# Optimization experiments

Hardware: AMD Instinct MI355X
Metric: run time of the kernel (lower is better)

## Reference

```python
import jax, jax.numpy as jnp
import numpy as np

NUM_CATEGORIES = 72
TEMPERATURE = 0.07
SEGMENT_WEIGHT = 10.0
MISSING_CATEGORIES = (13, 53, 61)
EPS = 1e-12
NEG_INF = -1e30


def setup_inputs() -> dict:
    key = jax.random.key(0)
    k1, k2 = jax.random.split(key)
    B, N, D = 4, 262144, 32
    embeddings = jax.random.normal(k1, (B, N, D), dtype=jnp.float32)
    segment_labels = jax.random.randint(k2, (B, N), 0, NUM_CATEGORIES, dtype=jnp.int64)
    return {"embeddings": embeddings, "segment_labels": segment_labels}


def _l2norm(x):
    return x / jnp.maximum(jnp.linalg.norm(x, axis=-1, keepdims=True), EPS)


def reference(embeddings, segment_labels):
    C = NUM_CATEGORIES
    missing = jnp.zeros((C,), dtype=bool).at[jnp.array(MISSING_CATEGORIES)].set(True)
    valid = segment_labels >= 0                      # [B,N]
    labels = jnp.clip(segment_labels, 0, C - 1)      # safe indices
    emb_n = _l2norm(embeddings)                      # [B,N,D]

    def per_batch(e, lab, v):
        w = v.astype(e.dtype)                                        # [N]
        counts = jax.ops.segment_sum(w, lab, num_segments=C)         # [C]
        sums = jax.ops.segment_sum(e * w[:, None], lab, num_segments=C)  # [C,D]
        protos = _l2norm(sums / jnp.maximum(counts, 1.0)[:, None])   # [C,D]
        present = (counts > 0) & (~missing)                          # [C]
        # similarity over all categories, mask absent/missing prototypes
        sim = jnp.einsum('nd,cd->nc', e, protos) / TEMPERATURE       # [N,C]
        logits = jnp.where(present[None, :], sim, NEG_INF)
        logp = jax.nn.log_softmax(logits, axis=-1)
        nll = -jnp.take_along_axis(logp, lab[:, None], axis=1)[:, 0]  # [N]
        keep = (v & (~missing[lab])).astype(e.dtype)                  # ignore_index=-100 analogue
        return jnp.sum(nll * keep) / jnp.maximum(jnp.sum(keep), 1.0)

    losses = jax.vmap(per_batch)(emb_n, labels, valid)  # [B]
    segment_loss = jnp.mean(losses)                     # segment_count == B here
    return SEGMENT_WEIGHT * segment_loss
```

## Files before the change

kernel.cpp:

```cpp
#include <hip/hip_runtime.h>
#include <hip/hip_bf16.h>

#define NCAT 72
#define NCATP 80
#define DIM 32
#define ROWS 36
#define BNUM 4
#define TEMP_INV (1.0f / 0.07f)
#define SEG_W 10.0f

#define WS_SUMS 0
#define WS_CNTS 9216
#define WS_PROT 9504
#define WS_NABS 19744
#define WS_LOSS 19748
#define WS_KEEP 19752
#define WS_TOTAL 19756

typedef __attribute__((ext_vector_type(8))) short short8v;
typedef __attribute__((ext_vector_type(4))) float f32x4;
typedef __attribute__((ext_vector_type(4))) unsigned u32x4;

__device__ __forceinline__ bool is_missing(int c) {
    return (c == 13) | (c == 53) | (c == 61);
}

__device__ __forceinline__ short f2bf_hi(float f, float* hi_f) {
    unsigned u = __float_as_uint(f);
    unsigned r = u + 0x7FFFu + ((u >> 16) & 1u);
    *hi_f = __uint_as_float(r & 0xFFFF0000u);
    return (short)(r >> 16);
}
__device__ __forceinline__ short f2bf(float f) {
    unsigned u = __float_as_uint(f);
    unsigned r = u + 0x7FFFu + ((u >> 16) & 1u);
    return (short)(r >> 16);
}

__device__ __forceinline__ unsigned cvtpk_bf16(float a, float b) {
    unsigned r;
    asm("v_cvt_pk_bf16_f32 %0, %1, %2" : "=v"(r) : "v"(a), "v"(b));
    return r;
}

template <int BPB>
__global__ __launch_bounds__(256) void k_accum(const float* __restrict__ emb,
                                               const int* __restrict__ lab,
                                               float* __restrict__ ws, int Nb) {
    __shared__ float s_acc[4][NCAT][ROWS];
    __shared__ float s_cnt[4][NCAT];
    __shared__ int   s_prb[4][NCAT];
    const int t = threadIdx.x;
    const int b = blockIdx.x / BPB;
    const int blk = blockIdx.x % BPB;
    const int w = t >> 6;
    const int g = (t >> 3) & 7;
    const int sub = t & 7;
    const int pofs = t >> 3;

    for (int i = t; i < 4 * NCAT * ROWS; i += 256) ((float*)s_acc)[i] = 0.f;
    for (int i = t; i < 4 * NCAT; i += 256) ((float*)s_cnt)[i] = 0.f;
    __syncthreads();

    float* accw = &s_acc[w][0][0];
    int* prbw = &s_prb[w][0];
    const float* eb = emb + (size_t)b * Nb * DIM;
    const int* lb = lab + (size_t)b * Nb;

    int p = blk * 32 + pofs;
    int l_cur = lb[p];
    float4 v_cur = ((const float4*)(eb + (size_t)p * DIM))[sub];

    for (int p0 = blk * 32; p0 < Nb; p0 += BPB * 32) {
        const int pn = p0 + BPB * 32 + pofs;
        int l_nxt = -1;
        float4 v_nxt = make_float4(0.f, 0.f, 0.f, 0.f);
        if (pn < Nb) {
            l_nxt = lb[pn];
            v_nxt = ((const float4*)(eb + (size_t)pn * DIM))[sub];
        }

        float ss = v_cur.x * v_cur.x + v_cur.y * v_cur.y +
                   v_cur.z * v_cur.z + v_cur.w * v_cur.w;
        ss += __shfl_xor(ss, 1);
        ss += __shfl_xor(ss, 2);
        ss += __shfl_xor(ss, 4);
        const float inv = 1.0f / fmaxf(sqrtf(ss), 1e-12f);
        const bool valid = (l_cur >= 0);
        const int lc = min(max(l_cur, 0), NCAT - 1);
        float4 u;
        u.x = v_cur.x * inv; u.y = v_cur.y * inv;
        u.z = v_cur.z * inv; u.w = v_cur.w * inv;

        if (valid && sub == 0) unsafeAtomicAdd(&s_cnt[w][lc], 1.0f);

        float* rowp = accw + lc * ROWS + sub * 4;
        bool active = valid;
        while (__any(active)) {
            asm volatile("" ::: "memory");
            if (active && sub == 0) prbw[lc] = g;
            int win = 0;
            if (active && sub == 0) win = (prbw[lc] == g) ? 1 : 0;
            const unsigned long long wb = __ballot(win);
            const bool iwin = active && ((wb >> (g * 8)) & 1ull);
            if (iwin) {
                float4* r4 = (float4*)rowp;
                float4 o = *r4;
                o.x += u.x; o.y += u.y; o.z += u.z; o.w += u.w;
                *r4 = o;
            }
            active = active && !iwin;
        }

        l_cur = l_nxt;
        v_cur = v_nxt;
    }
    __syncthreads();

    float* gs = ws + WS_SUMS + b * NCAT * DIM;
    for (int i = t; i < NCAT * DIM; i += 256) {
        const int c = i >> 5, d = i & 31;
        float val = s_acc[0][c][d] + s_acc[1][c][d] +
                    s_acc[2][c][d] + s_acc[3][c][d];
        if (val != 0.f) unsafeAtomicAdd(&gs[i], val);
    }
    if (t < NCAT) {
        float c = s_cnt[0][t] + s_cnt[1][t] + s_cnt[2][t] + s_cnt[3][t];
        if (c != 0.f) unsafeAtomicAdd(ws + WS_CNTS + b * NCAT + t, c);
    }
}

__global__ __launch_bounds__(256) void k_proto(float* __restrict__ ws) {
    const int b = blockIdx.x;
    __shared__ float s_np;
    if (threadIdx.x == 0) s_np = 0.f;
    __syncthreads();
    const float* gs = ws + WS_SUMS + b * NCAT * DIM;
    const float* gc = ws + WS_CNTS + b * NCAT;
    float* gp = ws + WS_PROT + b * NCATP * DIM;
    const int dd = threadIdx.x & 31;
    const int r0 = threadIdx.x >> 5;
    for (int c = r0; c < NCAT; c += 8) {
        float cnt = gc[c];
        float val = gs[c * DIM + dd] / fmaxf(cnt, 1.0f);
        float ss = val * val;
        #pragma unroll
        for (int m = 16; m >= 1; m >>= 1) ss += __shfl_xor(ss, m);
        float inv = 1.0f / fmaxf(sqrtf(ss), 1e-12f);
        const bool present = (cnt > 0.f) && !is_missing(c);
        gp[c * DIM + dd] = present ? val * inv : 0.f;
        if (dd == 0) unsafeAtomicAdd(&s_np, present ? 1.f : 0.f);
    }
    __syncthreads();
    if (threadIdx.x == 0) ws[WS_NABS + b] = (float)NCATP - s_np;
}

__device__ __forceinline__ void point_group(
    int pt, int l, const float* __restrict__ eb,
    const short8v phi[5], const short8v plo[5],
    float nabs, int sub, float& lacc, float& dacc, float& kacc)
{
    const float LOG2E = 1.4426950408889634f;
    const int lc = min(max(l, 0), NCAT - 1);

    const float4* ep = (const float4*)(eb + (size_t)pt * DIM + sub * 8);
    float4 a0 = ep[0], a1 = ep[1];

    float ea[8] = {a0.x, a0.y, a0.z, a0.w, a1.x, a1.y, a1.z, a1.w};
    u32x4 hw, lw;
    #pragma unroll
    for (int j = 0; j < 4; j++) {
        const float x0 = ea[2 * j], x1 = ea[2 * j + 1];
        const unsigned h = cvtpk_bf16(x0, x1);
        const float h0 = __uint_as_float(h << 16);
        const float h1 = __uint_as_float(h & 0xFFFF0000u);
        hw[j] = h;
        lw[j] = cvtpk_bf16(x0 - h0, x1 - h1);
    }
    const short8v ehi = __builtin_bit_cast(short8v, hw);
    const short8v elo = __builtin_bit_cast(short8v, lw);

    float ss = a0.x * a0.x + a0.y * a0.y + a0.z * a0.z + a0.w * a0.w +
               a1.x * a1.x + a1.y * a1.y + a1.z * a1.z + a1.w * a1.w;
    ss += __shfl_xor(ss, 16);
    ss += __shfl_xor(ss, 32);
    const float kk = (TEMP_INV * LOG2E) * __builtin_amdgcn_rsqf(fmaxf(ss, 1e-24f));

    const bool keep = (l >= 0) && !is_missing(lc);
    const int ltile = lc >> 4;
    const bool qm = keep && (((lc >> 2) & 3) == sub);

    float s = 0.f;
    #pragma unroll
    for (int n = 0; n < 5; n++) {
        f32x4 acc = {0.f, 0.f, 0.f, 0.f};
        acc = __builtin_amdgcn_mfma_f32_16x16x32_bf16(phi[n], ehi, acc, 0, 0, 0);
        acc = __builtin_amdgcn_mfma_f32_16x16x32_bf16(plo[n], ehi, acc, 0, 0, 0);
        acc = __builtin_amdgcn_mfma_f32_16x16x32_bf16(phi[n], elo, acc, 0, 0, 0);
        s += __builtin_amdgcn_exp2f(acc[0] * kk) + __builtin_amdgcn_exp2f(acc[1] * kk) +
             __builtin_amdgcn_exp2f(acc[2] * kk) + __builtin_amdgcn_exp2f(acc[3] * kk);
        if (qm && ltile == n) {
            const float d01 = (lc & 1) ? acc[1] : acc[0];
            const float d23 = (lc & 1) ? acc[3] : acc[2];
            dacc += kk * ((lc & 2) ? d23 : d01);
        }
    }
    s += __shfl_xor(s, 16);
    s += __shfl_xor(s, 32);
    s -= nabs;
    const float cl = __builtin_amdgcn_logf(s);
    if (keep && sub == 0) {
        lacc += cl;
        kacc += 1.f;
    }
}

template <int BPB>
__global__ __launch_bounds__(256, 4) void k_loss(const float* __restrict__ emb,
                                                 const int* __restrict__ lab,
                                                 const float* __restrict__ protos,
                                                 const float* __restrict__ nabsp,
                                                 float* __restrict__ lossout,
                                                 int Nb) {
    __shared__ float s_red[8];
    const int b = blockIdx.x / BPB;
    const int blk = blockIdx.x % BPB;
    const int t = threadIdx.x;
    const int lane = t & 63;
    const int wave = t >> 6;
    const int lid = lane & 15;
    const int sub = lane >> 4;

    const float* pp = protos + b * NCATP * DIM;
    const float nabs = nabsp[b];
    const float* eb = emb + (size_t)b * Nb * DIM;
    const int* lb = lab + (size_t)b * Nb;
    const float LN2 = 0.6931471805599453f;

    short8v phi[5], plo[5];
    #pragma unroll
    for (int n = 0; n < 5; n++) {
        const int cat = n * 16 + lid;
        const float4* qk = (const float4*)(pp + cat * DIM + sub * 8);
        float4 q0 = qk[0], q1 = qk[1];
        float qa[8] = {q0.x, q0.y, q0.z, q0.w, q1.x, q1.y, q1.z, q1.w};
        #pragma unroll
        for (int j = 0; j < 8; j++) {
            float hf;
            phi[n][j] = f2bf_hi(qa[j], &hf);
            plo[n][j] = f2bf(qa[j] - hf);
        }
    }

    float lacc = 0.f, dacc = 0.f, kacc = 0.f;

    #pragma unroll 1
    for (int p0 = (blk * 4 + wave) * 64; p0 < Nb; p0 += BPB * 4 * 64) {
        const int lv = lb[p0 + lane];
        const int l0 = __shfl(lv, lid);
        const int l1 = __shfl(lv, 16 + lid);
        const int l2 = __shfl(lv, 32 + lid);
        const int l3 = __shfl(lv, 48 + lid);
        point_group(p0 + lid,      l0, eb, phi, plo, nabs, sub, lacc, dacc, kacc);
        point_group(p0 + 16 + lid, l1, eb, phi, plo, nabs, sub, lacc, dacc, kacc);
        point_group(p0 + 32 + lid, l2, eb, phi, plo, nabs, sub, lacc, dacc, kacc);
        point_group(p0 + 48 + lid, l3, eb, phi, plo, nabs, sub, lacc, dacc, kacc);
    }

    float v = lacc - dacc;
    #pragma unroll
    for (int m = 32; m >= 1; m >>= 1) {
        v += __shfl_xor(v, m);
        kacc += __shfl_xor(kacc, m);
    }
    if (lane == 0) {
        s_red[wave] = v;
        s_red[4 + wave] = kacc;
    }
    __syncthreads();
    if (t == 0) {
        float a = s_red[0] + s_red[1] + s_red[2] + s_red[3];
        float k = s_red[4] + s_red[5] + s_red[6] + s_red[7];
        unsafeAtomicAdd(lossout + b, LN2 * a);
        unsafeAtomicAdd(lossout + BNUM + b, k);
    }
}

__global__ void k_final(const float* __restrict__ ws, float* __restrict__ out) {
    if (threadIdx.x == 0 && blockIdx.x == 0) {
        float s = 0.f;
        for (int b = 0; b < BNUM; b++) {
            float l = ws[WS_LOSS + b];
            float k = ws[WS_KEEP + b];
            s += l / fmaxf(k, 1.0f);
        }
        out[0] = SEG_W * (s / BNUM);
    }
}

extern "C" void kernel_launch(void* const* d_in, const int* in_sizes, int n_in,
                              void* d_out, int out_size, void* d_ws, size_t ws_size,
                              hipStream_t stream) {
    const float* emb = (const float*)d_in[0];
    const int* lab = (const int*)d_in[1];
    float* ws = (float*)d_ws;
    float* out = (float*)d_out;
    const int total_pts = in_sizes[1];
    const int Nb = total_pts / BNUM;

    hipMemsetAsync(d_ws, 0, WS_TOTAL * sizeof(float), stream);
    constexpr int BPB_ACC = 192;
    constexpr int BPB_LOSS = 256;
    k_accum<BPB_ACC><<<dim3(BNUM * BPB_ACC), dim3(256), 0, stream>>>(emb, lab, ws, Nb);
    k_proto<<<dim3(BNUM), dim3(256), 0, stream>>>(ws);
    k_loss<BPB_LOSS><<<dim3(BNUM * BPB_LOSS), dim3(256), 0, stream>>>(
        emb, lab, ws + WS_PROT, ws + WS_NABS, ws + WS_LOSS, Nb);
    k_final<<<1, 64, 0, stream>>>(ws, out);
}
```

Measured before the change: 116.1 us.

## Fold proto and final kernels into last-block epilogues; stage proto fragments in LDS

Drops the separate k_proto and k_final launches. The last block to finish k_accum (found with an atomic counter and thread fences) builds the normalized prototypes. The last block of k_loss computes the final scalar. k_loss also converts the prototype bf16 hi/lo fragments once per block into shared memory instead of holding them in registers per thread, which frees VGPRs and may improve occupancy. The cost is an extra LDS read per MFMA, and the prototype step now runs serially over four batches in a single block.

```diff
diff --git a/kernel.cpp b/kernel.cpp
--- a/kernel.cpp
+++ b/kernel.cpp
@@ -15,7 +15,9 @@
 #define WS_NABS 19744
 #define WS_LOSS 19748
 #define WS_KEEP 19752
-#define WS_TOTAL 19756
+#define WS_CTR1 19756
+#define WS_CTR2 19757
+#define WS_TOTAL 19760
 
 typedef __attribute__((ext_vector_type(8))) short short8v;
 typedef __attribute__((ext_vector_type(4))) float f32x4;
@@ -50,6 +52,8 @@
     __shared__ float s_acc[4][NCAT][ROWS];
     __shared__ float s_cnt[4][NCAT];
     __shared__ int   s_prb[4][NCAT];
+    __shared__ int   s_last;
+    __shared__ float s_np;
     const int t = threadIdx.x;
     const int b = blockIdx.x / BPB;
     const int blk = blockIdx.x % BPB;
@@ -128,36 +132,45 @@
         float c = s_cnt[0][t] + s_cnt[1][t] + s_cnt[2][t] + s_cnt[3][t];
         if (c != 0.f) unsafeAtomicAdd(ws + WS_CNTS + b * NCAT + t, c);
     }
-}
-
-__global__ __launch_bounds__(256) void k_proto(float* __restrict__ ws) {
-    const int b = blockIdx.x;
-    __shared__ float s_np;
-    if (threadIdx.x == 0) s_np = 0.f;
-    __syncthreads();
-    const float* gs = ws + WS_SUMS + b * NCAT * DIM;
-    const float* gc = ws + WS_CNTS + b * NCAT;
-    float* gp = ws + WS_PROT + b * NCATP * DIM;
-    const int dd = threadIdx.x & 31;
-    const int r0 = threadIdx.x >> 5;
-    for (int c = r0; c < NCAT; c += 8) {
-        float cnt = gc[c];
-        float val = gs[c * DIM + dd] / fmaxf(cnt, 1.0f);
-        float ss = val * val;
-        #pragma unroll
-        for (int m = 16; m >= 1; m >>= 1) ss += __shfl_xor(ss, m);
-        float inv = 1.0f / fmaxf(sqrtf(ss), 1e-12f);
-        const bool present = (cnt > 0.f) && !is_missing(c);
-        gp[c * DIM + dd] = present ? val * inv : 0.f;
-        if (dd == 0) unsafeAtomicAdd(&s_np, present ? 1.f : 0.f);
-    }
-    __syncthreads();
-    if (threadIdx.x == 0) ws[WS_NABS + b] = (float)NCATP - s_np;
+
+    __syncthreads();
+    if (t == 0) {
+        __threadfence();
+        unsigned old = atomicAdd((unsigned*)(ws + WS_CTR1), 1u);
+        s_last = (old == (unsigned)(gridDim.x - 1)) ? 1 : 0;
+    }
+    __syncthreads();
+    if (s_last) {
+        __threadfence();
+        const int dd = t & 31;
+        const int r0 = t >> 5;
+        for (int bb = 0; bb < BNUM; bb++) {
+            if (t == 0) s_np = 0.f;
+            __syncthreads();
+            const float* gs2 = ws + WS_SUMS + bb * NCAT * DIM;
+            const float* gc2 = ws + WS_CNTS + bb * NCAT;
+            float* gp2 = ws + WS_PROT + bb * NCATP * DIM;
+            for (int c = r0; c < NCAT; c += 8) {
+                float cnt = gc2[c];
+                float val = gs2[c * DIM + dd] / fmaxf(cnt, 1.0f);
+                float sq = val * val;
+                #pragma unroll
+                for (int m = 16; m >= 1; m >>= 1) sq += __shfl_xor(sq, m);
+                float inv2 = 1.0f / fmaxf(sqrtf(sq), 1e-12f);
+                const bool present = (cnt > 0.f) && !is_missing(c);
+                gp2[c * DIM + dd] = present ? val * inv2 : 0.f;
+                if (dd == 0) unsafeAtomicAdd(&s_np, present ? 1.f : 0.f);
+            }
+            __syncthreads();
+            if (t == 0) ws[WS_NABS + bb] = (float)NCATP - s_np;
+            __syncthreads();
+        }
+    }
 }
 
 __device__ __forceinline__ void point_group(
     int pt, int l, const float* __restrict__ eb,
-    const short8v phi[5], const short8v plo[5],
+    const u32x4 (*__restrict__ sf)[64], int lane,
     float nabs, int sub, float& lacc, float& dacc, float& kacc)
 {
     const float LOG2E = 1.4426950408889634f;
@@ -193,10 +206,12 @@
     float s = 0.f;
     #pragma unroll
     for (int n = 0; n < 5; n++) {
+        const short8v phn = __builtin_bit_cast(short8v, sf[n * 2][lane]);
+        const short8v pln = __builtin_bit_cast(short8v, sf[n * 2 + 1][lane]);
         f32x4 acc = {0.f, 0.f, 0.f, 0.f};
-        acc = __builtin_amdgcn_mfma_f32_16x16x32_bf16(phi[n], ehi, acc, 0, 0, 0);
-        acc = __builtin_amdgcn_mfma_f32_16x16x32_bf16(plo[n], ehi, acc, 0, 0, 0);
-        acc = __builtin_amdgcn_mfma_f32_16x16x32_bf16(phi[n], elo, acc, 0, 0, 0);
+        acc = __builtin_amdgcn_mfma_f32_16x16x32_bf16(phn, ehi, acc, 0, 0, 0);
+        acc = __builtin_amdgcn_mfma_f32_16x16x32_bf16(pln, ehi, acc, 0, 0, 0);
+        acc = __builtin_amdgcn_mfma_f32_16x16x32_bf16(phn, elo, acc, 0, 0, 0);
         s += __builtin_amdgcn_exp2f(acc[0] * kk) + __builtin_amdgcn_exp2f(acc[1] * kk) +
              __builtin_amdgcn_exp2f(acc[2] * kk) + __builtin_amdgcn_exp2f(acc[3] * kk);
         if (qm && ltile == n) {
@@ -221,8 +236,11 @@
                                                  const float* __restrict__ protos,
                                                  const float* __restrict__ nabsp,
                                                  float* __restrict__ lossout,
+                                                 float* __restrict__ out,
                                                  int Nb) {
+    __shared__ u32x4 s_frag[10][64];
     __shared__ float s_red[8];
+    __shared__ int s_last;
     const int b = blockIdx.x / BPB;
     const int blk = blockIdx.x % BPB;
     const int t = threadIdx.x;
@@ -237,20 +255,25 @@
     const int* lb = lab + (size_t)b * Nb;
     const float LN2 = 0.6931471805599453f;
 
-    short8v phi[5], plo[5];
-    #pragma unroll
-    for (int n = 0; n < 5; n++) {
-        const int cat = n * 16 + lid;
-        const float4* qk = (const float4*)(pp + cat * DIM + sub * 8);
-        float4 q0 = qk[0], q1 = qk[1];
-        float qa[8] = {q0.x, q0.y, q0.z, q0.w, q1.x, q1.y, q1.z, q1.w};
+    if (wave == 0) {
         #pragma unroll
-        for (int j = 0; j < 8; j++) {
-            float hf;
-            phi[n][j] = f2bf_hi(qa[j], &hf);
-            plo[n][j] = f2bf(qa[j] - hf);
-        }
-    }
+        for (int n = 0; n < 5; n++) {
+            const int cat = n * 16 + lid;
+            const float4* qk = (const float4*)(pp + cat * DIM + sub * 8);
+            float4 q0 = qk[0], q1 = qk[1];
+            float qa[8] = {q0.x, q0.y, q0.z, q0.w, q1.x, q1.y, q1.z, q1.w};
+            short8v hi8, lo8;
+            #pragma unroll
+            for (int j = 0; j < 8; j++) {
+                float hf;
+                hi8[j] = f2bf_hi(qa[j], &hf);
+                lo8[j] = f2bf(qa[j] - hf);
+            }
+            s_frag[n * 2][lane] = __builtin_bit_cast(u32x4, hi8);
+            s_frag[n * 2 + 1][lane] = __builtin_bit_cast(u32x4, lo8);
+        }
+    }
+    __syncthreads();
 
     float lacc = 0.f, dacc = 0.f, kacc = 0.f;
 
@@ -261,10 +284,10 @@
         const int l1 = __shfl(lv, 16 + lid);
         const int l2 = __shfl(lv, 32 + lid);
         const int l3 = __shfl(lv, 48 + lid);
-        point_group(p0 + lid,      l0, eb, phi, plo, nabs, sub, lacc, dacc, kacc);
-        point_group(p0 + 16 + lid, l1, eb, phi, plo, nabs, sub, lacc, dacc, kacc);
-        point_group(p0 + 32 + lid, l2, eb, phi, plo, nabs, sub, lacc, dacc, kacc);
-        point_group(p0 + 48 + lid, l3, eb, phi, plo, nabs, sub, lacc, dacc, kacc);
+        point_group(p0 + lid,      l0, eb, s_frag, lane, nabs, sub, lacc, dacc, kacc);
+        point_group(p0 + 16 + lid, l1, eb, s_frag, lane, nabs, sub, lacc, dacc, kacc);
+        point_group(p0 + 32 + lid, l2, eb, s_frag, lane, nabs, sub, lacc, dacc, kacc);
+        point_group(p0 + 48 + lid, l3, eb, s_frag, lane, nabs, sub, lacc, dacc, kacc);
     }
 
     float v = lacc - dacc;
@@ -283,16 +306,18 @@
         float k = s_red[4] + s_red[5] + s_red[6] + s_red[7];
         unsafeAtomicAdd(lossout + b, LN2 * a);
         unsafeAtomicAdd(lossout + BNUM + b, k);
-    }
-}
-
-__global__ void k_final(const float* __restrict__ ws, float* __restrict__ out) {
-    if (threadIdx.x == 0 && blockIdx.x == 0) {
+        __threadfence();
+        unsigned old = atomicAdd((unsigned*)(lossout + (WS_CTR2 - WS_LOSS)), 1u);
+        s_last = (old == (unsigned)(gridDim.x - 1)) ? 1 : 0;
+    }
+    __syncthreads();
+    if (s_last && t == 0) {
+        __threadfence();
         float s = 0.f;
-        for (int b = 0; b < BNUM; b++) {
-            float l = ws[WS_LOSS + b];
-            float k = ws[WS_KEEP + b];
-            s += l / fmaxf(k, 1.0f);
+        for (int b2 = 0; b2 < BNUM; b2++) {
+            float l = lossout[b2];
+            float k2 = lossout[BNUM + b2];
+            s += l / fmaxf(k2, 1.0f);
         }
         out[0] = SEG_W * (s / BNUM);
     }
@@ -312,8 +337,6 @@
     constexpr int BPB_ACC = 192;
     constexpr int BPB_LOSS = 256;
     k_accum<BPB_ACC><<<dim3(BNUM * BPB_ACC), dim3(256), 0, stream>>>(emb, lab, ws, Nb);
-    k_proto<<<dim3(BNUM), dim3(256), 0, stream>>>(ws);
     k_loss<BPB_LOSS><<<dim3(BNUM * BPB_LOSS), dim3(256), 0, stream>>>(
-        emb, lab, ws + WS_PROT, ws + WS_NABS, ws + WS_LOSS, Nb);
-    k_final<<<1, 64, 0, stream>>>(ws, out);
-}
+        emb, lab, ws + WS_PROT, ws + WS_NABS, ws + WS_LOSS, out, Nb);
+}
```

After: 152.9 us. 1.32x slower.
